# Optimization experiments

Measured on AMD Instinct MI355X. Metric: run time of the kernel, lower is better.

Reference implementation:

```python
import jax, jax.numpy as jnp
import numpy as np

B, IN, ED, PW, OUT, CL, NK = 2048, 4096, 8192, 2048, 256, 16, 32
MIX = 0.5

def _onehot_mask(key, n):
    # near-one-hot selector matrix [n, NK], as built by forward_update_masks
    idx = jax.random.choice(key, n, (NK,), replace=False)
    return jnp.zeros((n, NK), jnp.float32).at[idx, jnp.arange(NK)].set(1.0)

def setup_inputs():
    ks = jax.random.split(jax.random.key(0), 24)
    f = jnp.float32
    adj = (jax.random.uniform(ks[4], (IN, IN)) < 0.01).astype(f)
    adj = jnp.maximum(adj, adj.T).at[jnp.arange(IN), jnp.arange(IN)].set(1.0)
    return {
        'x_gene': jax.random.normal(ks[0], (B, IN), f),
        'x_invmea': jax.random.normal(ks[1], (B, IN), f),
        'x_curv': jax.random.normal(ks[2], (B, ED), f),
        'clinn': jax.random.normal(ks[3], (B, CL), f),
        'Adj': adj,
        'edge_mask': (jax.random.uniform(ks[5], (ED, IN)) < 0.005).astype(f),
        'pathway_mask': (jax.random.uniform(ks[6], (PW, ED)) < 0.02).astype(f),
        'top_gene_mask': _onehot_mask(ks[7], IN),
        'top_invmea_mask': _onehot_mask(ks[8], IN),
        'top_curv_mask': _onehot_mask(ks[9], ED),
        'top_path_mask': _onehot_mask(ks[10], PW),
        'W1': jnp.full((IN, IN), 0.05, f),
        'b1': 0.01 * jax.random.normal(ks[11], (IN,), f),
        'W2': jnp.full((ED, IN), 0.05, f),
        'b2': 0.01 * jax.random.normal(ks[12], (ED,), f),
        'W3': jnp.full((PW, ED), 0.05, f),
        'b3': 0.01 * jax.random.normal(ks[13], (PW,), f),
        'W4': 0.02 * jax.random.normal(ks[14], (OUT, PW), f),
        'b4': 0.01 * jax.random.normal(ks[15], (OUT,), f),
        'W5': 0.02 * jax.random.normal(ks[16], (OUT, OUT), f),
        'b5': 0.01 * jax.random.normal(ks[17], (OUT,), f),
        'W6': 0.05 * jax.random.normal(ks[18], (OUT, OUT + CL + 4 * NK), f),
        'W7': 0.05 * jax.random.normal(ks[19], (1, OUT), f),
        'mp11': MIX * jnp.ones(IN, f),
        'mp12': (1.0 - MIX) * jnp.ones(IN, f),
        'mp1': jnp.ones(IN, f),
        'mp21': MIX * jnp.ones(ED, f),
        'mp22': (1.0 - MIX) * jnp.ones(ED, f),
        'mp2': jnp.ones(ED, f),
        'mp3': jnp.ones(PW, f),
    }

def reference(x_gene, x_invmea, x_curv, clinn, Adj, edge_mask, pathway_mask,
              top_gene_mask, top_invmea_mask, top_curv_mask, top_path_mask,
              W1, b1, W2, b2, W3, b3, W4, b4, W5, b5, W6, W7,
              mp11, mp12, mp1, mp21, mp22, mp2, mp3):
    sg = jax.lax.stop_gradient
    sig = jax.nn.sigmoid
    kept_gene = sg(x_gene @ top_gene_mask)                     # [B,NK] gather-as-matmul
    x1 = sig(x_gene @ (W1 * Adj).T + b1)                       # masked linear [B,IN]
    x1 = x_invmea * (mp11 * mp1) + x1 * (mp12 * mp1)
    kept_invmea = sg(x1 @ top_invmea_mask)
    x1 = sig(x1 @ (W2 * edge_mask).T + b2)                     # [B,ED]
    x1 = x_curv * (mp21 * mp2) + x1 * (mp22 * mp2)
    kept_curv = sg(x1 @ top_curv_mask)
    x1 = sig(x1 @ (W3 * pathway_mask).T + b3)                  # [B,PW]
    x1 = x1 * mp3
    kept_path = sg(x1 @ top_path_mask)
    x1 = sig(x1 @ W4.T + b4)
    x1 = sig(x1 @ W5.T + b5)                                   # [B,OUT]
    x_cat = jnp.concatenate([x1, kept_gene, kept_invmea, kept_curv, kept_path, clinn], axis=1)
    lp = sig(x_cat @ W6.T)
    lp = lp - jnp.mean(lp, axis=1, keepdims=True)
    return lp @ W7.T                                           # [B,1]
```

## Files before the change

### kernel.cpp

```cpp
#include <hip/hip_runtime.h>

typedef unsigned short u16;
typedef __attribute__((ext_vector_type(4))) float f32x4;
typedef __attribute__((ext_vector_type(8))) short s16x8;

__device__ __forceinline__ u16 f2bf(float f) {
    union { float f; unsigned u; } c; c.f = f;
    return (u16)((c.u + 0x7fffu + ((c.u >> 16) & 1u)) >> 16);
}
__device__ __forceinline__ float bf2f(u16 u) {
    union { unsigned u; float f; } c; c.u = ((unsigned)u) << 16; return c.f;
}
__device__ __forceinline__ unsigned pk2(float a, float b) {
    return (unsigned)f2bf(a) | ((unsigned)f2bf(b) << 16);
}
__device__ __forceinline__ float sigm(float x) { return 1.0f / (1.0f + __expf(-x)); }
__device__ __forceinline__ void fma2(unsigned xv, float w, float& a0, float& a1) {
    union { float f; unsigned u; } lo, hi;
    lo.u = xv << 16; hi.u = xv & 0xFFFF0000u;
    a0 += w * lo.f; a1 += w * hi.f;
}

__device__ __forceinline__ void load16_g2l(const void* g, void* l) {
    __builtin_amdgcn_global_load_lds(
        (const __attribute__((address_space(1))) unsigned int*)(unsigned long long)g,
        (__attribute__((address_space(3))) unsigned int*)(unsigned int)(unsigned long long)l,
        16, 0, 0);
}

__device__ void d_transpF(const float* __restrict__ in, u16* __restrict__ out,
                          int Rr, int Cc, int bx, int by, float (*t)[65]) {
    const int r0 = by * 64, c0 = bx * 64;
    const int tid = threadIdx.x;
#pragma unroll
    for (int i = 0; i < 16; i++) {
        int idx = tid + i * 256;
        int rr = idx >> 6, cc = idx & 63;
        t[rr][cc] = in[(size_t)(r0 + rr) * Cc + c0 + cc];
    }
    __syncthreads();
#pragma unroll
    for (int i = 0; i < 16; i++) {
        int idx = tid + i * 256;
        int cc = idx >> 6, rr = idx & 63;
        out[(size_t)(c0 + cc) * Rr + r0 + rr] = f2bf(t[rr][cc]);
    }
}

__device__ void d_find(const float* __restrict__ mask, int n, int* __restrict__ outp,
                       int* red, int k) {
    int best = -1;
    for (int i = threadIdx.x; i < n; i += 256)
        if (mask[(size_t)i * 32 + k] != 0.0f) best = i;
    red[threadIdx.x] = best;
    __syncthreads();
    for (int off = 128; off > 0; off >>= 1) {
        if (threadIdx.x < off) {
            int o = red[threadIdx.x + off];
            if (o > red[threadIdx.x]) red[threadIdx.x] = o;
        }
        __syncthreads();
    }
    if (threadIdx.x == 0) *outp = red[0] < 0 ? 0 : red[0];
}

__device__ void d_conv(const float* __restrict__ in, u16* __restrict__ out,
                       int bid, unsigned n8) {
    unsigned i = bid * 256u + threadIdx.x;
    if (i >= n8) return;
    float4 a = ((const float4*)in)[2 * i];
    float4 b = ((const float4*)in)[2 * i + 1];
    uint4 o;
    o.x = pk2(a.x, a.y); o.y = pk2(a.z, a.w);
    o.z = pk2(b.x, b.y); o.w = pk2(b.z, b.w);
    ((uint4*)out)[i] = o;
}

template <int CHUNKS>
__device__ void d_ell_reg(const float* __restrict__ M, const float* __restrict__ W,
                          unsigned* __restrict__ ell, int* __restrict__ cnt,
                          int PAD, int R, int bid) {
    const int lane = threadIdx.x & 63;
    const int row = bid * 4 + (threadIdx.x >> 6);
    if (row >= R) return;
    const int C = CHUNKS * 2048;
    const float4* mrow = (const float4*)(M + (size_t)row * C);
    const float4* wrow = (const float4*)(W + (size_t)row * C);
    unsigned* erow = ell + (size_t)row * PAD;
    int base = 0;
#pragma unroll
    for (int hh = 0; hh < CHUNKS * 2; hh++) {
        float4 m[4];
#pragma unroll
        for (int i = 0; i < 4; i++) m[i] = mrow[hh * 256 + lane + i * 64];
        unsigned bits = 0;
#pragma unroll
        for (int i = 0; i < 4; i++) {
            if (m[i].x != 0.f) bits |= 1u << (4 * i);
            if (m[i].y != 0.f) bits |= 2u << (4 * i);
            if (m[i].z != 0.f) bits |= 4u << (4 * i);
            if (m[i].w != 0.f) bits |= 8u << (4 * i);
        }
        __builtin_amdgcn_sched_barrier(0);
        float4 w[4];
#pragma unroll
        for (int i = 0; i < 4; i++)
            if ((bits >> (4 * i)) & 0xFu) w[i] = wrow[hh * 256 + lane + i * 64];
        __asm__ volatile("" ::: "memory");

        const int n = __popc(bits);
        int pre = n;
#pragma unroll
        for (int off = 1; off < 64; off <<= 1) {
            int t = __shfl_up(pre, off, 64);
            if (lane >= off) pre += t;
        }
        int s = base + pre - n;
#pragma unroll
        for (int i = 0; i < 4; i++) {
            if ((bits >> (4 * i)) & 0xFu) {
                int c = hh * 1024 + lane * 4 + i * 256;
                if (bits & (1u << (4 * i))) { if (s < PAD) erow[s] = ((unsigned)f2bf(w[i].x) << 16) | (unsigned)(c + 0); s++; }
                if (bits & (2u << (4 * i))) { if (s < PAD) erow[s] = ((unsigned)f2bf(w[i].y) << 16) | (unsigned)(c + 1); s++; }
                if (bits & (4u << (4 * i))) { if (s < PAD) erow[s] = ((unsigned)f2bf(w[i].z) << 16) | (unsigned)(c + 2); s++; }
                if (bits & (8u << (4 * i))) { if (s < PAD) erow[s] = ((unsigned)f2bf(w[i].w) << 16) | (unsigned)(c + 3); s++; }
            }
        }
        base += __shfl(pre, 63, 64);
    }
    if (lane == 0) cnt[row] = base > PAD ? PAD : base;
}

__global__ __launch_bounds__(256, 8) void prep_all(
    const float* __restrict__ Adj, const float* __restrict__ W1,
    unsigned* __restrict__ ell1, int* __restrict__ cnt1,
    const float* __restrict__ edge, const float* __restrict__ W2,
    unsigned* __restrict__ ell2, int* __restrict__ cnt2,
    const float* __restrict__ path, const float* __restrict__ W3,
    unsigned* __restrict__ ell3, int* __restrict__ cnt3,
    const float* __restrict__ xg_f, const float* __restrict__ xinv_f,
    const float* __restrict__ xcv_f,
    u16* __restrict__ xTg, u16* __restrict__ xinvT, u16* __restrict__ xcvT,
    const float* __restrict__ m0, const float* __restrict__ m1,
    const float* __restrict__ m2, const float* __restrict__ m3,
    int* __restrict__ idx,
    const float* __restrict__ W4, u16* __restrict__ w4b,
    const float* __restrict__ W5, u16* __restrict__ w5b) {
    __shared__ float tile[64][65];
    const long long T = 12192, E = 3584;
    const int b = blockIdx.x;
    const int ea = (int)(((long long)b * E) / T);
    const int eb = (int)(((long long)(b + 1) * E) / T);
    if (eb > ea) {
        int id = ea;
        if (id < 1024) { d_ell_reg<2>(Adj, W1, ell1, cnt1, 256, 4096, id); return; }
        id -= 1024;
        if (id < 2048) { d_ell_reg<2>(edge, W2, ell2, cnt2, 96, 8192, id); return; }
        d_ell_reg<4>(path, W3, ell3, cnt3, 320, 2048, id - 2048);
        return;
    }
    int id = b - ea;
    if (id < 2048) { d_transpF(xg_f, xTg, 2048, 4096, id & 63, id >> 6, tile); return; }
    id -= 2048;
    if (id < 2048) { d_transpF(xinv_f, xinvT, 2048, 4096, id & 63, id >> 6, tile); return; }
    id -= 2048;
    if (id < 4096) { d_transpF(xcv_f, xcvT, 2048, 8192, id & 127, id >> 7, tile); return; }
    id -= 4096;
    if (id < 128) {
        const float* mk; int n;
        int which = id >> 5;
        if (which == 0)      { mk = m0; n = 4096; }
        else if (which == 1) { mk = m1; n = 4096; }
        else if (which == 2) { mk = m2; n = 8192; }
        else                 { mk = m3; n = 2048; }
        d_find(mk, n, idx + which * 32 + (id & 31), (int*)tile, id & 31);
        return;
    }
    id -= 128;
    if (id < 256) { d_conv(W4, w4b, id, 65536u); return; }
    id -= 256;
    d_conv(W5, w5b, id, 8192u);
}

template <int BPL>
__global__ __launch_bounds__(256) void spmm(const unsigned* __restrict__ ell,
                                            const int* __restrict__ cnt,
                                            const u16* __restrict__ xT,
                                            u16* __restrict__ outT,
                                            const float* __restrict__ bias,
                                            const float* __restrict__ c1a,
                                            const float* __restrict__ c1b,
                                            const float* __restrict__ c2a,
                                            const float* __restrict__ c2b,
                                            const u16* __restrict__ invT,
                                            const int* __restrict__ gidx,
                                            u16* __restrict__ gdst,
                                            int PAD) {
    const int lane = threadIdx.x & 63;
    const int wv = __builtin_amdgcn_readfirstlane((int)(threadIdx.x >> 6));
    const int j = blockIdx.y * 4 + wv;
    const int b0 = blockIdx.x * (64 * BPL) + lane * BPL;

    const unsigned* ep = ell + (size_t)j * PAD;
    int len = cnt[j];
    if (len > PAD) len = PAD;

    float acc[BPL];
#pragma unroll
    for (int i = 0; i < BPL; i++) acc[i] = 0.f;

    const int nfull = len >> 3;
    unsigned eA[8];
    if (nfull > 0) {
#pragma unroll
        for (int t = 0; t < 8; t++) eA[t] = ep[t];
    }
    for (int g = 0; g < nfull; g++) {
        unsigned eB[8];
        const bool more = (g + 1 < nfull);
        if (more) {
#pragma unroll
            for (int t = 0; t < 8; t++) eB[t] = ep[(g + 1) * 8 + t];
        }
        if (BPL == 8) {
            uint4 xv[8];
#pragma unroll
            for (int t = 0; t < 8; t++)
                xv[t] = *(const uint4*)(xT + ((size_t)(eA[t] & 0xFFFFu) << 11) + b0);
#pragma unroll
            for (int t = 0; t < 8; t++) {
                union { float f; unsigned u; } w; w.u = (eA[t] >> 16) << 16;
                fma2(xv[t].x, w.f, acc[0], acc[1]);
                fma2(xv[t].y, w.f, acc[2], acc[3]);
                fma2(xv[t].z, w.f, acc[4], acc[5]);
                fma2(xv[t].w, w.f, acc[6], acc[7]);
            }
        } else {
            uint2 xv[8];
#pragma unroll
            for (int t = 0; t < 8; t++)
                xv[t] = *(const uint2*)(xT + ((size_t)(eA[t] & 0xFFFFu) << 11) + b0);
#pragma unroll
            for (int t = 0; t < 8; t++) {
                union { float f; unsigned u; } w; w.u = (eA[t] >> 16) << 16;
                fma2(xv[t].x, w.f, acc[0], acc[1]);
                fma2(xv[t].y, w.f, acc[2], acc[3]);
            }
        }
        if (more) {
#pragma unroll
            for (int t = 0; t < 8; t++) eA[t] = eB[t];
        }
    }
    for (int s = nfull * 8; s < len; ++s) {
        unsigned e = ep[s];
        union { float f; unsigned u; } w; w.u = (e >> 16) << 16;
        const u16* xp = xT + ((size_t)(e & 0xFFFFu) << 11) + b0;
        if (BPL == 8) {
            uint4 xv = *(const uint4*)xp;
            fma2(xv.x, w.f, acc[0], acc[1]); fma2(xv.y, w.f, acc[2], acc[3]);
            fma2(xv.z, w.f, acc[4], acc[5]); fma2(xv.w, w.f, acc[6], acc[7]);
        } else {
            uint2 xv = *(const uint2*)xp;
            fma2(xv.x, w.f, acc[0], acc[1]); fma2(xv.y, w.f, acc[2], acc[3]);
        }
    }

    const float bi = bias[j];
    float c1 = 0.f;
    if (c1a) { c1 = c1a[j]; if (c1b) c1 *= c1b[j]; }
    float c2 = 1.f;
    if (c2a) { c2 = c2a[j]; if (c2b) c2 *= c2b[j]; }

    float v[BPL];
#pragma unroll
    for (int i = 0; i < BPL; i++) v[i] = sigm(acc[i] + bi) * c2;
    if (invT) {
        const unsigned long long* ip = (const unsigned long long*)(invT + ((size_t)j << 11) + b0);
#pragma unroll
        for (int h = 0; h < BPL / 4; h++) {
            unsigned long long iv = __builtin_nontemporal_load(ip + h);
            unsigned lo = (unsigned)iv, hi = (unsigned)(iv >> 32);
            union { float f; unsigned u; } g0, g1, g2, g3;
            g0.u = lo << 16; g1.u = lo & 0xFFFF0000u;
            g2.u = hi << 16; g3.u = hi & 0xFFFF0000u;
            v[4 * h + 0] += g0.f * c1; v[4 * h + 1] += g1.f * c1;
            v[4 * h + 2] += g2.f * c1; v[4 * h + 3] += g3.f * c1;
        }
    }
    unsigned long long pkv[BPL / 4];
#pragma unroll
    for (int h = 0; h < BPL / 4; h++)
        pkv[h] = (unsigned long long)pk2(v[4 * h + 0], v[4 * h + 1])
               | ((unsigned long long)pk2(v[4 * h + 2], v[4 * h + 3]) << 32);
    unsigned long long* op = (unsigned long long*)(outT + ((size_t)j << 11) + b0);
#pragma unroll
    for (int h = 0; h < BPL / 4; h++) __builtin_nontemporal_store(pkv[h], op + h);

    if (gdst) {
        for (int t = 0; t < 32; t++) {
            if (gidx[t] == j) {
                unsigned long long* gp = (unsigned long long*)(gdst + t * 2048 + b0);
#pragma unroll
                for (int h = 0; h < BPL / 4; h++) gp[h] = pkv[h];
            }
        }
    }
}

__global__ __launch_bounds__(256) void gatherFT(const float* __restrict__ src, int ld,
                                                const int* __restrict__ idx,
                                                u16* __restrict__ dstT) {
    int i = blockIdx.x * 256 + threadIdx.x;
    int kk = i >> 11, b = i & 2047;
    dstT[i] = f2bf(src[(size_t)b * ld + idx[kk]]);
}

__global__ __launch_bounds__(256) void transpB(const u16* __restrict__ in,
                                               u16* __restrict__ out, int Rr, int Cc) {
    __shared__ u16 t[64][66];
    const int r0 = blockIdx.y * 64, c0 = blockIdx.x * 64;
    const int tid = threadIdx.x;
#pragma unroll
    for (int i = 0; i < 16; i++) {
        int idx = tid + i * 256;
        int rr = idx >> 6, cc = idx & 63;
        t[rr][cc] = in[(size_t)(r0 + rr) * Cc + c0 + cc];
    }
    __syncthreads();
#pragma unroll
    for (int i = 0; i < 16; i++) {
        int idx = tid + i * 256;
        int cc = idx >> 6, rr = idx & 63;
        out[(size_t)(c0 + cc) * Rr + r0 + rr] = t[rr][cc];
    }
}

template <int WR, int WC, int MF, int NF, int KC, int WPE>
__global__ __launch_bounds__(WR * WC * 64, WPE)
void gemm_t(const u16* __restrict__ A, const u16* __restrict__ W,
            u16* __restrict__ Out, const float* __restrict__ bias, int N, int K) {
    constexpr int NTHR = WR * WC * 64;
    constexpr int BM = WR * MF * 16;
    constexpr int BN = WC * NF * 16;
    constexpr int BK = KC * 32;
    constexpr int CPR = KC * 4;
    constexpr int MSK = CPR - 1;
    constexpr int CA = BM * CPR / NTHR;
    constexpr int CB = BN * CPR / NTHR;
    constexpr int L  = CA + CB;

    __shared__ u16 At[2][BM * BK];
    __shared__ u16 Bt[2][BN * BK];

    const int tid = threadIdx.x;
    const int lane = tid & 63;
    const int wave = tid >> 6;
    const int wr = wave / WC, wc = wave % WC;
    const int tn = blockIdx.x, tm = blockIdx.y;
    const int r16 = lane & 15;
    const int q = lane >> 4;

    const u16* aSrc[CA]; int aDst[CA];
#pragma unroll
    for (int j = 0; j < CA; j++) {
        int c = tid + j * NTHR;
        int r = c / CPR, p = c - r * CPR;
        aSrc[j] = A + (size_t)(tm * BM + r) * K + (p ^ (r & MSK)) * 8;
        aDst[j] = c * 8;
    }
    const u16* bSrc[CB]; int bDst[CB];
#pragma unroll
    for (int j = 0; j < CB; j++) {
        int c = tid + j * NTHR;
        int r = c / CPR, p = c - r * CPR;
        bSrc[j] = W + (size_t)(tn * BN + r) * K + (p ^ (r & MSK)) * 8;
        bDst[j] = c * 8;
    }
    int aRd[MF][KC], bRd[NF][KC];
#pragma unroll
    for (int mi = 0; mi < MF; mi++)
#pragma unroll
        for (int kc = 0; kc < KC; kc++)
            aRd[mi][kc] = (wr * MF * 16 + mi * 16 + r16) * BK + (((kc * 4 + q) ^ (r16 & MSK)) << 3);
#pragma unroll
    for (int ni = 0; ni < NF; ni++)
#pragma unroll
        for (int kc = 0; kc < KC; kc++)
            bRd[ni][kc] = (wc * NF * 16 + ni * 16 + r16) * BK + (((kc * 4 + q) ^ (r16 & MSK)) << 3);

    const int nIter = K / BK;

#define ISSUE(slot, it_)                                              \
    do {                                                              \
        const int k0_ = (it_) * BK;                                   \
        _Pragma("unroll")                                             \
        for (int j = 0; j < CA; j++)                                  \
            load16_g2l(aSrc[j] + k0_, &At[slot][aDst[j]]);            \
        _Pragma("unroll")                                             \
        for (int j = 0; j < CB; j++)                                  \
            load16_g2l(bSrc[j] + k0_, &Bt[slot][bDst[j]]);            \
    } while (0)

    ISSUE(0, 0);
    if (nIter > 1) ISSUE(1, 1);

    f32x4 acc[MF][NF];
#pragma unroll
    for (int i = 0; i < MF; i++)
#pragma unroll
        for (int j = 0; j < NF; j++) acc[i][j] = (f32x4){0.f, 0.f, 0.f, 0.f};

    for (int it = 0; it < nIter; ++it) {
        const int s = it & 1;
        if (it + 1 < nIter) __builtin_amdgcn_s_waitcnt(0xF70 | L);
        else                __builtin_amdgcn_s_waitcnt(0xF70);
        __asm__ volatile("" ::: "memory");
        __builtin_amdgcn_s_barrier();
        __asm__ volatile("" ::: "memory");

        s16x8 af[KC][MF], bfr[KC][NF];
#pragma unroll
        for (int kc = 0; kc < KC; kc++) {
#pragma unroll
            for (int mi = 0; mi < MF; mi++) af[kc][mi] = *(const s16x8*)(&At[s][aRd[mi][kc]]);
#pragma unroll
            for (int ni = 0; ni < NF; ni++) bfr[kc][ni] = *(const s16x8*)(&Bt[s][bRd[ni][kc]]);
        }
        __asm__ volatile("" ::: "memory");
        __builtin_amdgcn_s_waitcnt(0xC07F);
        __builtin_amdgcn_s_barrier();
        __asm__ volatile("" ::: "memory");

        if (it + 2 < nIter) ISSUE(s, it + 2);

#pragma unroll
        for (int kc = 0; kc < KC; kc++)
#pragma unroll
            for (int mi = 0; mi < MF; mi++)
#pragma unroll
                for (int ni = 0; ni < NF; ni++)
                    acc[mi][ni] = __builtin_amdgcn_mfma_f32_16x16x32_bf16(af[kc][mi], bfr[kc][ni], acc[mi][ni], 0, 0, 0);
    }
#undef ISSUE

#pragma unroll
    for (int ni = 0; ni < NF; ni++) {
        const int n = tn * BN + wc * NF * 16 + ni * 16 + r16;
        const float bi = bias ? bias[n] : 0.f;
#pragma unroll
        for (int mi = 0; mi < MF; mi++) {
#pragma unroll
            for (int rg = 0; rg < 4; rg++) {
                const int m = tm * BM + wr * MF * 16 + mi * 16 + q * 4 + rg;
                Out[(size_t)m * N + n] = f2bf(sigm(acc[mi][ni][rg] + bi));
            }
        }
    }
}

__global__ __launch_bounds__(256) void tail_k(const u16* __restrict__ x5,
                                              const u16* __restrict__ kgT,
                                              const u16* __restrict__ kiT,
                                              const u16* __restrict__ kcT,
                                              const u16* __restrict__ kpT,
                                              const float* __restrict__ clinn,
                                              const float* __restrict__ W6,
                                              const float* __restrict__ W7,
                                              float* __restrict__ out) {
    __shared__ float xs[8 * 400];
    __shared__ float s1[4][8], s2[4][8], s3[4];
    const int tid = threadIdx.x;
    const int b0 = blockIdx.x * 8;
    for (int i = tid; i < 8 * 400; i += 256) {
        int r = i / 400, c = i - r * 400;
        int b = b0 + r;
        float v;
        if (c < 256)      v = bf2f(x5[b * 256 + c]);
        else if (c < 288) v = bf2f(kgT[(c - 256) * 2048 + b]);
        else if (c < 320) v = bf2f(kiT[(c - 288) * 2048 + b]);
        else if (c < 352) v = bf2f(kcT[(c - 320) * 2048 + b]);
        else if (c < 384) v = bf2f(kpT[(c - 352) * 2048 + b]);
        else              v = clinn[b * 16 + (c - 384)];
        xs[i] = v;
    }
    __syncthreads();
    const int j = tid;
    float acc[8];
#pragma unroll
    for (int r = 0; r < 8; r++) acc[r] = 0.f;
    const float4* wrow = (const float4*)(W6 + (size_t)j * 400);
    for (int c = 0; c < 100; c++) {
        float4 wv = wrow[c];
        const float* wp = (const float*)&wv;
#pragma unroll
        for (int t = 0; t < 4; t++) {
            float w = wp[t];
            int k = c * 4 + t;
#pragma unroll
            for (int r = 0; r < 8; r++) acc[r] += w * xs[r * 400 + k];
        }
    }
    const float w7j = W7[j];
    const int lane = tid & 63, wave = tid >> 6;
    float t3 = w7j;
#pragma unroll
    for (int off = 32; off > 0; off >>= 1) t3 += __shfl_down(t3, off, 64);
    if (lane == 0) s3[wave] = t3;
#pragma unroll
    for (int r = 0; r < 8; r++) {
        float lp = sigm(acc[r]);
        float t1 = lp, t2 = lp * w7j;
#pragma unroll
        for (int off = 32; off > 0; off >>= 1) {
            t1 += __shfl_down(t1, off, 64);
            t2 += __shfl_down(t2, off, 64);
        }
        if (lane == 0) { s1[wave][r] = t1; s2[wave][r] = t2; }
    }
    __syncthreads();
    if (tid < 8) {
        float S1 = s1[0][tid] + s1[1][tid] + s1[2][tid] + s1[3][tid];
        float S2 = s2[0][tid] + s2[1][tid] + s2[2][tid] + s2[3][tid];
        float SW = s3[0] + s3[1] + s3[2] + s3[3];
        out[b0 + tid] = S2 - (S1 * (1.f / 256.f)) * SW;
    }
}

extern "C" void kernel_launch(void* const* d_in, const int* in_sizes, int n_in,
                              void* d_out, int out_size, void* d_ws, size_t ws_size,
                              hipStream_t stream) {
    const float* x_gene   = (const float*)d_in[0];
    const float* x_invmea = (const float*)d_in[1];
    const float* x_curv   = (const float*)d_in[2];
    const float* clinn    = (const float*)d_in[3];
    const float* Adj      = (const float*)d_in[4];
    const float* edge_m   = (const float*)d_in[5];
    const float* path_m   = (const float*)d_in[6];
    const float* tg_mask  = (const float*)d_in[7];
    const float* ti_mask  = (const float*)d_in[8];
    const float* tc_mask  = (const float*)d_in[9];
    const float* tp_mask  = (const float*)d_in[10];
    const float* W1 = (const float*)d_in[11];  const float* b1 = (const float*)d_in[12];
    const float* W2 = (const float*)d_in[13];  const float* b2 = (const float*)d_in[14];
    const float* W3 = (const float*)d_in[15];  const float* b3 = (const float*)d_in[16];
    const float* W4 = (const float*)d_in[17];  const float* b4 = (const float*)d_in[18];
    const float* W5 = (const float*)d_in[19];  const float* b5 = (const float*)d_in[20];
    const float* W6 = (const float*)d_in[21];
    const float* W7 = (const float*)d_in[22];
    const float* mp11 = (const float*)d_in[23];
    const float* mp12 = (const float*)d_in[24];
    const float* mp1  = (const float*)d_in[25];
    const float* mp21 = (const float*)d_in[26];
    const float* mp22 = (const float*)d_in[27];
    const float* mp2  = (const float*)d_in[28];
    const float* mp3  = (const float*)d_in[29];

    char* ws = (char*)d_ws;
    const float* nulf = nullptr;
    float* out = (float*)d_out;

    u16*  xTg   = (u16*)(ws + 0);
    u16*  xinvT = (u16*)(ws + 16777216);
    u16*  xcvT  = (u16*)(ws + 33554432);
    u16*  x1T   = (u16*)(ws + 67108864);
    u16*  x2T   = (u16*)(ws + 83886080);
    u16*  x3T   = (u16*)(ws + 117440512);
    u16*  x3    = (u16*)(ws + 125829120);
    unsigned* ell1 = (unsigned*)(ws + 134217728);
    unsigned* ell2 = (unsigned*)(ws + 138412032);
    unsigned* ell3 = (unsigned*)(ws + 141557760);
    int* cnt1 = (int*)(ws + 144179200);
    int* cnt2 = (int*)(ws + 144195584);
    int* cnt3 = (int*)(ws + 144228352);
    int* idxg = (int*)(ws + 144236544);
    int* idxi = idxg + 32;
    int* idxc = idxg + 64;
    int* idxp = idxg + 96;
    u16* kgT  = (u16*)(ws + 144237056);
    u16* kiT  = (u16*)(ws + 144368128);
    u16* kcT  = (u16*)(ws + 144499200);
    u16* kpT  = (u16*)(ws + 144630272);
    u16* w4b  = (u16*)(ws + 144761344);
    u16* w5b  = (u16*)(ws + 145809920);
    u16* x4   = (u16*)(ws + 145940992);
    u16* x5   = (u16*)(ws + 146989568);

    prep_all<<<12192, 256, 0, stream>>>(
        Adj, W1, ell1, cnt1, edge_m, W2, ell2, cnt2, path_m, W3, ell3, cnt3,
        x_gene, x_invmea, x_curv, xTg, xinvT, xcvT,
        tg_mask, ti_mask, tc_mask, tp_mask, idxg, W4, w4b, W5, w5b);
    gatherFT<<<256, 256, 0, stream>>>(x_gene, 4096, idxg, kgT);

    spmm<4><<<dim3(8, 1024), 256, 0, stream>>>(ell1, cnt1, xTg, x1T, b1,
                                               mp11, mp1, mp12, mp1, xinvT,
                                               idxi, kiT, 256);
    spmm<4><<<dim3(8, 2048), 256, 0, stream>>>(ell2, cnt2, x1T, x2T, b2,
                                               mp21, mp2, mp22, mp2, xcvT,
                                               idxc, kcT, 96);
    spmm<4><<<dim3(8, 512), 256, 0, stream>>>(ell3, cnt3, x2T, x3T, b3,
                                              nulf, nulf, mp3, nulf, (const u16*)nullptr,
                                              idxp, kpT, 320);
    transpB<<<dim3(32, 32), 256, 0, stream>>>(x3T, x3, 2048, 2048);

    gemm_t<2, 2, 2, 2, 2, 4><<<dim3(4, 32), 256, 0, stream>>>(x3, w4b, x4, b4, 256, 2048);
    gemm_t<2, 2, 2, 2, 2, 4><<<dim3(4, 32), 256, 0, stream>>>(x4, w5b, x5, b5, 256, 256);

    tail_k<<<256, 256, 0, stream>>>(x5, kgT, kiT, kcT, kpT, clinn, W6, W7, out);
}
```

Before: 896.8 us.

## Split ELL row compaction across four waves per block with LDS prefix

```diff
diff --git a/kernel.cpp b/kernel.cpp
--- a/kernel.cpp
+++ b/kernel.cpp
@@ -76,62 +76,82 @@
     ((uint4*)out)[i] = o;
 }
 
-template <int CHUNKS>
-__device__ void d_ell_reg(const float* __restrict__ M, const float* __restrict__ W,
+template <int SUBC>
+__device__ void d_ell_row(const float* __restrict__ M, const float* __restrict__ W,
                           unsigned* __restrict__ ell, int* __restrict__ cnt,
-                          int PAD, int R, int bid) {
+                          int PAD, int row, int* __restrict__ lds) {
     const int lane = threadIdx.x & 63;
-    const int row = bid * 4 + (threadIdx.x >> 6);
-    if (row >= R) return;
-    const int C = CHUNKS * 2048;
+    const int wv = threadIdx.x >> 6;
+    const int C = SUBC * 4096;
     const float4* mrow = (const float4*)(M + (size_t)row * C);
     const float4* wrow = (const float4*)(W + (size_t)row * C);
     unsigned* erow = ell + (size_t)row * PAD;
+
+    float4 m[SUBC * 4];
+#pragma unroll
+    for (int k = 0; k < SUBC * 4; k++) {
+        int sc = k >> 2, i = k & 3;
+        m[k] = mrow[(wv * SUBC + sc) * 256 + lane + i * 64];
+    }
+    unsigned bits[SUBC];
+    int total = 0;
+#pragma unroll
+    for (int sc = 0; sc < SUBC; sc++) {
+        unsigned b = 0;
+#pragma unroll
+        for (int i = 0; i < 4; i++) {
+            const float4 mm = m[sc * 4 + i];
+            if (mm.x != 0.f) b |= 1u << (4 * i);
+            if (mm.y != 0.f) b |= 2u << (4 * i);
+            if (mm.z != 0.f) b |= 4u << (4 * i);
+            if (mm.w != 0.f) b |= 8u << (4 * i);
+        }
+        bits[sc] = b;
+        total += __popc(b);
+    }
+    float4 w[SUBC * 4];
+#pragma unroll
+    for (int k = 0; k < SUBC * 4; k++) {
+        int sc = k >> 2, i = k & 3;
+        if ((bits[sc] >> (4 * i)) & 0xFu)
+            w[k] = wrow[(wv * SUBC + sc) * 256 + lane + i * 64];
+    }
+    int pre = total;
+#pragma unroll
+    for (int off = 1; off < 64; off <<= 1) {
+        int t = __shfl_up(pre, off, 64);
+        if (lane >= off) pre += t;
+    }
+    if (lane == 63) lds[wv] = pre;
+    __syncthreads();
     int base = 0;
 #pragma unroll
-    for (int hh = 0; hh < CHUNKS * 2; hh++) {
-        float4 m[4];
-#pragma unroll
-        for (int i = 0; i < 4; i++) m[i] = mrow[hh * 256 + lane + i * 64];
-        unsigned bits = 0;
+    for (int v = 0; v < 3; v++) if (v < wv) base += lds[v];
+    int s = base + pre - total;
+    __asm__ volatile("" ::: "memory");
+#pragma unroll
+    for (int sc = 0; sc < SUBC; sc++) {
+        const unsigned b = bits[sc];
+        const int f4b = (wv * SUBC + sc) * 256;
 #pragma unroll
         for (int i = 0; i < 4; i++) {
-            if (m[i].x != 0.f) bits |= 1u << (4 * i);
-            if (m[i].y != 0.f) bits |= 2u << (4 * i);
-            if (m[i].z != 0.f) bits |= 4u << (4 * i);
-            if (m[i].w != 0.f) bits |= 8u << (4 * i);
-        }
-        __builtin_amdgcn_sched_barrier(0);
-        float4 w[4];
-#pragma unroll
-        for (int i = 0; i < 4; i++)
-            if ((bits >> (4 * i)) & 0xFu) w[i] = wrow[hh * 256 + lane + i * 64];
-        __asm__ volatile("" ::: "memory");
-
-        const int n = __popc(bits);
-        int pre = n;
-#pragma unroll
-        for (int off = 1; off < 64; off <<= 1) {
-            int t = __shfl_up(pre, off, 64);
-            if (lane >= off) pre += t;
-        }
-        int s = base + pre - n;
-#pragma unroll
-        for (int i = 0; i < 4; i++) {
-            if ((bits >> (4 * i)) & 0xFu) {
-                int c = hh * 1024 + lane * 4 + i * 256;
-                if (bits & (1u << (4 * i))) { if (s < PAD) erow[s] = ((unsigned)f2bf(w[i].x) << 16) | (unsigned)(c + 0); s++; }
-                if (bits & (2u << (4 * i))) { if (s < PAD) erow[s] = ((unsigned)f2bf(w[i].y) << 16) | (unsigned)(c + 1); s++; }
-                if (bits & (4u << (4 * i))) { if (s < PAD) erow[s] = ((unsigned)f2bf(w[i].z) << 16) | (unsigned)(c + 2); s++; }
-                if (bits & (8u << (4 * i))) { if (s < PAD) erow[s] = ((unsigned)f2bf(w[i].w) << 16) | (unsigned)(c + 3); s++; }
+            if ((b >> (4 * i)) & 0xFu) {
+                const float4 wv4 = w[sc * 4 + i];
+                int c = (f4b + lane + i * 64) * 4;
+                if (b & (1u << (4 * i))) { if (s < PAD) erow[s] = ((unsigned)f2bf(wv4.x) << 16) | (unsigned)(c + 0); s++; }
+                if (b & (2u << (4 * i))) { if (s < PAD) erow[s] = ((unsigned)f2bf(wv4.y) << 16) | (unsigned)(c + 1); s++; }
+                if (b & (4u << (4 * i))) { if (s < PAD) erow[s] = ((unsigned)f2bf(wv4.z) << 16) | (unsigned)(c + 2); s++; }
+                if (b & (8u << (4 * i))) { if (s < PAD) erow[s] = ((unsigned)f2bf(wv4.w) << 16) | (unsigned)(c + 3); s++; }
             }
         }
-        base += __shfl(pre, 63, 64);
-    }
-    if (lane == 0) cnt[row] = base > PAD ? PAD : base;
-}
-
-__global__ __launch_bounds__(256, 8) void prep_all(
+    }
+    if (threadIdx.x == 0) {
+        int rt = lds[0] + lds[1] + lds[2] + lds[3];
+        cnt[row] = rt > PAD ? PAD : rt;
+    }
+}
+
+__global__ __launch_bounds__(256) void prep_all(
     const float* __restrict__ Adj, const float* __restrict__ W1,
     unsigned* __restrict__ ell1, int* __restrict__ cnt1,
     const float* __restrict__ edge, const float* __restrict__ W2,
@@ -147,16 +167,16 @@
     const float* __restrict__ W4, u16* __restrict__ w4b,
     const float* __restrict__ W5, u16* __restrict__ w5b) {
     __shared__ float tile[64][65];
-    const long long T = 12192, E = 3584;
+    const long long T = 22944, E = 14336;
     const int b = blockIdx.x;
     const int ea = (int)(((long long)b * E) / T);
     const int eb = (int)(((long long)(b + 1) * E) / T);
     if (eb > ea) {
         int id = ea;
-        if (id < 1024) { d_ell_reg<2>(Adj, W1, ell1, cnt1, 256, 4096, id); return; }
-        id -= 1024;
-        if (id < 2048) { d_ell_reg<2>(edge, W2, ell2, cnt2, 96, 8192, id); return; }
-        d_ell_reg<4>(path, W3, ell3, cnt3, 320, 2048, id - 2048);
+        if (id < 4096) { d_ell_row<1>(Adj, W1, ell1, cnt1, 256, id, (int*)tile); return; }
+        id -= 4096;
+        if (id < 8192) { d_ell_row<1>(edge, W2, ell2, cnt2, 96, id, (int*)tile); return; }
+        d_ell_row<2>(path, W3, ell3, cnt3, 320, id - 8192, (int*)tile);
         return;
     }
     int id = b - ea;
@@ -586,7 +606,7 @@
     u16* x4   = (u16*)(ws + 145940992);
     u16* x5   = (u16*)(ws + 146989568);
 
-    prep_all<<<12192, 256, 0, stream>>>(
+    prep_all<<<22944, 256, 0, stream>>>(
         Adj, W1, ell1, cnt1, edge_m, W2, ell2, cnt2, path_m, W3, ell3, cnt3,
         x_gene, x_invmea, x_curv, xTg, xinvT, xcvT,
         tg_mask, ti_mask, tc_mask, tp_mask, idxg, W4, w4b, W5, w5b);
```

New measurement: 870.8 us. 2.9% less time.
